# Performance work log

Hardware: AMD Instinct MI355X
Metric: run time of the kernel (lower is better)

The kernel has to match this reference:

```python
import jax, jax.numpy as jnp
import numpy as np
import math

B, S, D, H = 4, 1024, 1024, 16
HD = D // H  # 64
DFF = 4 * D
LN_EPS = 1e-5

def setup_inputs() -> dict:
    key = jax.random.key(0)
    ks = jax.random.split(key, 24)
    sd = lambda fi, fo: 1.0 / math.sqrt(fi)
    def lin(k, fi, fo):
        k1, k2 = jax.random.split(k)
        w = jax.random.uniform(k1, (fi, fo), jnp.float32, -sd(fi, fo), sd(fi, fo))
        b = jax.random.uniform(k2, (fo,), jnp.float32, -sd(fi, fo), sd(fi, fo))
        return w, b
    x = jax.random.normal(ks[0], (B, S, D), jnp.float32)
    Wk, bk = lin(ks[1], D, D)
    Wq, bq = lin(ks[2], D, D)
    Wv, bv = lin(ks[3], D, D)
    # per-head projections stacked over heads: [H, D, HD]
    def head_lin(k):
        kk = jax.random.split(k, H)
        ws, bs = zip(*[lin(kk[h], D, HD) for h in range(H)])
        return jnp.stack(ws), jnp.stack(bs)
    Whq, bhq = head_lin(ks[4])
    Whk, bhk = head_lin(ks[5])
    Whv, bhv = head_lin(ks[6])
    Wo, bo = lin(ks[7], D, D)
    W1, b1 = lin(ks[8], D, DFF)
    W2, b2 = lin(ks[9], DFF, D)
    gamma = jnp.ones((D,), jnp.float32)
    beta = jnp.zeros((D,), jnp.float32)
    return dict(x=x, Wk=Wk, bk=bk, Wq=Wq, bq=bq, Wv=Wv, bv=bv,
                Whq=Whq, bhq=bhq, Whk=Whk, bhk=bhk, Whv=Whv, bhv=bhv,
                Wo=Wo, bo=bo, W1=W1, b1=b1, W2=W2, b2=b2,
                gamma=gamma, beta=beta)

def _layer_norm(x, gamma, beta):
    mu = jnp.mean(x, axis=-1, keepdims=True)
    var = jnp.mean(jnp.square(x - mu), axis=-1, keepdims=True)
    return (x - mu) * jax.lax.rsqrt(var + LN_EPS) * gamma + beta

def reference(x, Wk, bk, Wq, bq, Wv, bv, Whq, bhq, Whk, bhk, Whv, bhv,
              Wo, bo, W1, b1, W2, b2, gamma, beta):
    # outer projections; NOTE: forward passes (k, q, v) into MHA, so the
    # MHA 'Q' stream is k_proj(x), 'K' stream is q_proj(x), 'V' is v_proj(x)
    ko = x @ Wk + bk
    qo = x @ Wq + bq
    vo = x @ Wv + bv
    # per-head projections (batched over heads): [B,H,S,HD]
    q = jnp.einsum('bsd,hde->bhse', ko, Whq) + bhq[None, :, None, :]
    k = jnp.einsum('bsd,hde->bhse', qo, Whk) + bhk[None, :, None, :]
    v = jnp.einsum('bsd,hde->bhse', vo, Whv) + bhv[None, :, None, :]
    # NOTE: original scales by sqrt(d_model), not sqrt(head_dim)
    scores = jnp.einsum('bhse,bhte->bhst', q, k) / math.sqrt(D)
    w = jax.nn.softmax(scores, axis=-1)
    o = jnp.einsum('bhst,bhte->bhse', w, v)         # [B,H,S,HD]
    o = o.transpose(0, 2, 1, 3).reshape(B, S, D)    # concat heads
    attn = o @ Wo + bo
    # dropout is identity in eval; shared LayerNorm after both residuals
    r1 = _layer_norm(x + attn, gamma, beta)
    ff = jax.nn.gelu(r1 @ W1 + b1, approximate=False) @ W2 + b2
    out = _layer_norm(r1 + ff, gamma, beta)
    return out
```

## Files before the change

kernel.cpp:

```cpp
#include <hip/hip_runtime.h>
#include <cstdint>
#include <cstddef>

#define D_MODEL 1024
#define SEQ 1024
#define BATCH 4
#define NHEAD 16
#define HDIM 64
#define ROWS (BATCH*SEQ)

typedef unsigned short u16;
typedef __attribute__((ext_vector_type(4))) unsigned short u16x4;
typedef __attribute__((ext_vector_type(8))) unsigned short u16x8;
typedef __attribute__((ext_vector_type(8))) __bf16 bf16x8v;
typedef __attribute__((ext_vector_type(4))) float f32x4;

__device__ inline u16 f2bf(float f){
  union{float f; unsigned u;} c; c.f = f;
  unsigned r = c.u + 0x7FFFu + ((c.u>>16)&1u);
  return (u16)(r>>16);
}
__device__ inline float bf2f(u16 s){
  union{unsigned u; float f;} c; c.u = ((unsigned)s)<<16; return c.f;
}
__device__ inline float gelu_f(float x){ return 0.5f*x*(1.f+erff(x*0.7071067811865475f)); }

__device__ __forceinline__ void gload_lds16(const void* g, void* l){
  __builtin_amdgcn_global_load_lds(
    (const __attribute__((address_space(1))) unsigned int*)g,
    (__attribute__((address_space(3))) unsigned int*)l, 16, 0, 0);
}

__global__ __launch_bounds__(256) void convert_bf(const float* __restrict__ in, u16* __restrict__ out){
  size_t idx = (size_t)blockIdx.x*256 + threadIdx.x;
  f32x4 v = *(const f32x4*)(in + idx*4);
  u16x4 o = { f2bf(v.x), f2bf(v.y), f2bf(v.z), f2bf(v.w) };
  *(u16x4*)(out + idx*4) = o;
}

__global__ __launch_bounds__(256) void transpose_conv(const float* __restrict__ W, u16* __restrict__ WT, int K, int N){
  __shared__ float tile[32][33];
  int n0 = blockIdx.x*32, k0 = blockIdx.y*32;
  int tx = threadIdx.x & 31, ty = threadIdx.x >> 5;
  #pragma unroll
  for (int i=0;i<4;i++){
    int r = ty + i*8;
    tile[r][tx] = W[(size_t)(k0+r)*N + n0 + tx];
  }
  __syncthreads();
  #pragma unroll
  for (int i=0;i<4;i++){
    int r = ty + i*8;
    WT[(size_t)(n0+r)*K + k0 + tx] = f2bf(tile[tx][r]);
  }
}

__global__ __launch_bounds__(256) void head_transpose(const float* __restrict__ Wh, u16* __restrict__ WT){
  __shared__ float tile[32][33];
  int d0 = blockIdx.x*32, e0 = blockIdx.y*32, h = blockIdx.z;
  int tx = threadIdx.x & 31, ty = threadIdx.x >> 5;
  #pragma unroll
  for (int i=0;i<4;i++){
    int r = ty + i*8;
    tile[r][tx] = Wh[(size_t)h*D_MODEL*HDIM + (size_t)(d0+r)*HDIM + e0 + tx];
  }
  __syncthreads();
  #pragma unroll
  for (int i=0;i<4;i++){
    int r = ty + i*8;
    WT[(size_t)(h*HDIM + e0 + r)*D_MODEL + d0 + tx] = f2bf(tile[tx][r]);
  }
}

__global__ __launch_bounds__(256) void bias_cat(const float* a, const float* b, const float* c, float* o){
  int i = blockIdx.x*256 + threadIdx.x;
  float v = (i < 1024) ? a[i] : (i < 2048) ? b[i-1024] : c[i-2048];
  o[i] = v;
}

__global__ __launch_bounds__(512,2) void gemm256_8p(
  const u16* __restrict__ A, const u16* __restrict__ BT, const float* __restrict__ bias,
  u16* __restrict__ outB, int N, int K, int mode, int act)
{
  __shared__ __align__(16) u16 As[2][2][128*64];
  __shared__ __align__(16) u16 Bs[2][2][128*64];
  int t = threadIdx.x, lane = t&63, wid = t>>6;
  int wr = wid>>2, wc = wid&3;
  int fr = lane&15, kg = lane>>4;
  int gx = gridDim.x;
  int bid = blockIdx.y*gx + blockIdx.x;
  int nwg = gx*gridDim.y;
  int cpx = nwg>>3;
  int sw = (bid&7)*cpx + (bid>>3);
  int tc = sw % gx, tr = sw / gx;

  const u16* Abase = A  + (size_t)tr*256*K;
  const u16* Bbase = BT + (size_t)tc*256*K;
  int srow = lane>>3, sch8 = lane&7;

  f32x4 acc[8][4];
  #pragma unroll
  for (int m=0;m<8;m++)
    #pragma unroll
    for (int n=0;n<4;n++) acc[m][n] = (f32x4)0.f;

  bf16x8v af[2][4], bfv[2][2];

  #define STAGE_A8(buf,h,kt) { _Pragma("unroll") for (int li=0;li<2;li++){ \
    int sr = (wid*2+li)*8 + srow; \
    int gr = ((sr>>6)<<7) + (h)*64 + (sr&63); \
    int sc = sch8 ^ (sr&7); \
    gload_lds16(Abase + (size_t)gr*K + (size_t)(kt)*64 + sc*8, &As[buf][h][(wid*2+li)*512]); } }
  #define STAGE_B8(buf,h,kt) { _Pragma("unroll") for (int li=0;li<2;li++){ \
    int sr = (wid*2+li)*8 + srow; \
    int gc = ((sr>>5)<<6) + (h)*32 + (sr&31); \
    int sc = sch8 ^ (sr&7); \
    gload_lds16(Bbase + (size_t)gc*K + (size_t)(kt)*64 + sc*8, &Bs[buf][h][(wid*2+li)*512]); } }
  #define LDA8(buf,h) { _Pragma("unroll") for (int ks=0;ks<2;ks++) _Pragma("unroll") for (int mf=0;mf<4;mf++){ \
    int r = wr*64 + mf*16 + fr; \
    af[ks][mf] = *(const bf16x8v*)&As[buf][h][r*64 + (((kg+4*ks)^(r&7)))*8]; } }
  #define LDB8(buf,h) { _Pragma("unroll") for (int ks=0;ks<2;ks++) _Pragma("unroll") for (int nf=0;nf<2;nf++){ \
    int r = wc*32 + nf*16 + fr; \
    bfv[ks][nf] = *(const bf16x8v*)&Bs[buf][h][r*64 + (((kg+4*ks)^(r&7)))*8]; } }
  #define MM8(mq,nq) { asm volatile("s_waitcnt lgkmcnt(0)" ::: "memory"); \
    __builtin_amdgcn_s_setprio(1); \
    _Pragma("unroll") for (int ks=0;ks<2;ks++) _Pragma("unroll") for (int mf=0;mf<4;mf++) _Pragma("unroll") for (int nf=0;nf<2;nf++) \
      acc[(mq)*4+mf][(nq)*2+nf] = __builtin_amdgcn_mfma_f32_16x16x32_bf16(af[ks][mf], bfv[ks][nf], acc[(mq)*4+mf][(nq)*2+nf], 0,0,0); \
    __builtin_amdgcn_s_setprio(0); }
  #define BAR asm volatile("s_barrier" ::: "memory")

  int NT = K >> 6;
  STAGE_A8(0,0,0); STAGE_B8(0,0,0); STAGE_B8(0,1,0); STAGE_A8(0,1,0);
  asm volatile("s_waitcnt vmcnt(4)" ::: "memory");
  BAR;

  for (int kt=0; kt<NT; ++kt){
    int buf = kt&1, nb = buf^1;
    int pre = (kt+1 < NT);
    LDA8(buf,0); LDB8(buf,0);
    if (pre){ STAGE_A8(nb,0,kt+1); asm volatile("s_waitcnt vmcnt(4)" ::: "memory"); }
    else    {                      asm volatile("s_waitcnt vmcnt(2)" ::: "memory"); }
    BAR; MM8(0,0); BAR;
    LDB8(buf,1);
    if (pre){ STAGE_B8(nb,0,kt+1); asm volatile("s_waitcnt vmcnt(4)" ::: "memory"); }
    else    {                      asm volatile("s_waitcnt vmcnt(0)" ::: "memory"); }
    BAR; MM8(0,1); BAR;
    LDA8(buf,1);
    if (pre){ STAGE_B8(nb,1,kt+1); asm volatile("s_waitcnt vmcnt(6)" ::: "memory"); }
    BAR; MM8(1,1); BAR;
    LDB8(buf,0);
    if (pre){ STAGE_A8(nb,1,kt+1); asm volatile("s_waitcnt vmcnt(4)" ::: "memory"); }
    BAR; MM8(1,0); BAR;
  }

  int crow0 = tr*256 + wr*128;
  int ccol0 = tc*256 + wc*64;
  #pragma unroll
  for (int n=0;n<4;n++){
    int col = ccol0 + n*16 + fr;
    float bv = bias[mode==0 ? col : (col & (N-1))];
    #pragma unroll
    for (int m=0;m<8;m++){
      int rbase = crow0 + m*16 + kg*4;
      #pragma unroll
      for (int i=0;i<4;i++){
        float v = acc[m][n][i] + bv;
        if (act) v = gelu_f(v);
        int row = rbase + i;
        if (mode == 0)
          outB[(size_t)(col>>10)*((size_t)ROWS*1024) + (size_t)row*1024 + (col&1023)] = f2bf(v);
        else
          outB[(size_t)row*N + col] = f2bf(v);
      }
    }
  }
}

__device__ __forceinline__ void stage128(u16 (*As)[4096], u16 (*Bs)[4096], int b,
  const u16* Ab, const u16* Bb, int Kstride, int kt, int wid, int rr, int sch)
{
  #pragma unroll
  for (int c=0;c<2;c++){
    int reg = c*4 + wid;
    int row = reg*16 + rr;
    gload_lds16(Ab + (size_t)row*Kstride + kt*32 + sch*8, &As[b][reg*512]);
  }
  #pragma unroll
  for (int c=0;c<2;c++){
    int reg = c*4 + wid;
    int row = reg*16 + rr;
    gload_lds16(Bb + (size_t)row*Kstride + kt*32 + sch*8, &Bs[b][reg*512]);
  }
}

__device__ __forceinline__ void gemm128_core(u16 (*As)[4096], u16 (*Bs)[4096],
  const u16* __restrict__ A, const u16* __restrict__ BT, const float* __restrict__ bias,
  float* __restrict__ outF, u16* __restrict__ outB,
  int N, int Kstride, int kofs, int Ksub, int mode, int act, int addbias)
{
  int t = threadIdx.x, lane = t&63, wid = t>>6;
  int wr = wid>>1, wc = wid&1;
  int fr = lane&15, kg = lane>>4;
  int gx = gridDim.x;
  int bid = blockIdx.y*gx + blockIdx.x;
  int nwg = gx*gridDim.y;
// ... 33 lines not shown
    for (int m=0;m<4;m++){
      int r = wr*64 + m*16 + fr;
      af[m] = *(const bf16x8v*)&As[buf][r*32 + (kg ^ ((r>>1)&3))*8];
    }
    #pragma unroll
    for (int n=0;n<4;n++){
      int r = wc*64 + n*16 + fr;
      bfv[n] = *(const bf16x8v*)&Bs[buf][r*32 + (kg ^ ((r>>1)&3))*8];
    }
    #pragma unroll
    for (int m=0;m<4;m++)
      #pragma unroll
      for (int n=0;n<4;n++)
        acc[m][n] = __builtin_amdgcn_mfma_f32_16x16x32_bf16(af[m], bfv[n], acc[m][n], 0,0,0);
    if (kt+1 < NT)
      asm volatile("s_barrier" ::: "memory");
    buf += 1; if (buf >= 3) buf = 0;
  }

  int crow0 = tr*128 + wr*64;
  int ccol0 = tc*128 + wc*64;
  #pragma unroll
  for (int n=0;n<4;n++){
    int col = ccol0 + n*16 + fr;
    float bv = addbias ? bias[col] : 0.f;
    #pragma unroll
    for (int m=0;m<4;m++){
      int rbase = crow0 + m*16 + kg*4;
      #pragma unroll
      for (int i=0;i<4;i++){
        float v = acc[m][n][i] + bv;
        if (act) v = gelu_f(v);
        int row = rbase + i;
        if (mode == 0){
          outB[(size_t)(col>>10)*((size_t)ROWS*1024) + (size_t)row*1024 + (col&1023)] = f2bf(v);
        } else if (mode == 1){
          outB[(size_t)row*N + col] = f2bf(v);
        } else if (mode == 2){
          int b = row >> 10, s = row & 1023;
          int h = col >> 6, e = col & 63;
          outB[(((size_t)((b*NHEAD + h)*HDIM + e))<<10) + s] = f2bf(v);
        } else {
          outF[(size_t)row*1024 + col] = v;
        }
      }
    }
  }
}

__global__ __launch_bounds__(256) void g_gemm_sk(
  const u16* A, const u16* BT, const float* bias, float* outBase, int K)
{
  __shared__ __align__(16) u16 As[3][4096];
  __shared__ __align__(16) u16 Bs[3][4096];
  int z = blockIdx.z;
  int Ksub = K >> 1;
  gemm128_core(As, Bs, A, BT, bias, outBase + (size_t)z*ROWS*1024, nullptr,
               1024, K, z*Ksub, Ksub, 3, 0, z==0);
}

struct B3 { const u16* A[3]; const u16* BT[3]; const float* bias[3]; u16* Cb[3]; int mode[3]; };
__global__ __launch_bounds__(256) void g_gemm_b3(B3 p){
  __shared__ __align__(16) u16 As[3][4096];
  __shared__ __align__(16) u16 Bs[3][4096];
  int z = blockIdx.z;
  gemm128_core(As, Bs, p.A[z], p.BT[z], p.bias[z], nullptr, p.Cb[z],
               1024, 1024, 0, 1024, p.mode[z], 0, 1);
}

__global__ __launch_bounds__(256) void attn_mfma(const u16* __restrict__ Q, const u16* __restrict__ Km,
                                                 const u16* __restrict__ Vt, u16* __restrict__ O)
{
  __shared__ __align__(16) u16 Ks[64*64];
  __shared__ __align__(16) u16 Vs[64*64];
  __shared__ __align__(16) u16 Ps[4][16*64];
  int t = threadIdx.x, lane = t & 63, wid = t >> 6;
  int fr = lane & 15, kg = lane >> 4;
  int qt = blockIdx.x, h = blockIdx.y, b = blockIdx.z;
  const size_t qkbase = ((size_t)b*SEQ)*D_MODEL + (size_t)h*HDIM;
  const size_t vtb = ((size_t)(b*NHEAD + h))*HDIM*SEQ;

  int qrow = qt*64 + wid*16 + fr;
  bf16x8v aq[2];
  aq[0] = *(const bf16x8v*)(Q + qkbase + (size_t)qrow*D_MODEL + kg*8);
  aq[1] = *(const bf16x8v*)(Q + qkbase + (size_t)qrow*D_MODEL + 32 + kg*8);

  f32x4 Oacc[4];
  #pragma unroll
  for (int n=0;n<4;n++) Oacc[n] = (f32x4)0.f;
  float m_run[4], l_run[4];
  #pragma unroll
  for (int i=0;i<4;i++){ m_run[i] = -3e38f; l_run[i] = 0.f; }

  int srow = lane >> 3;
  int sch  = (lane & 7) ^ srow;
  int x7 = fr & 7;

  for (int kt = 0; kt < SEQ/64; ++kt){
    #pragma unroll
    for (int c=0;c<2;c++){
      int r0 = (wid*2 + c)*8;
      int rowk = r0 + srow;
      gload_lds16(Km + qkbase + (size_t)(kt*64 + rowk)*D_MODEL + sch*8, &Ks[r0*64]);
      gload_lds16(Vt + vtb + (size_t)rowk*SEQ + kt*64 + sch*8, &Vs[r0*64]);
    }
    __syncthreads();

    f32x4 z4 = (f32x4)0.f;
    f32x4 s4[4];
    #pragma unroll
    for (int n=0;n<4;n++){
      int r = n*16 + fr;
      bf16x8v k0v = *(const bf16x8v*)&Ks[r*64 + ((kg  ) ^ x7)*8];
      bf16x8v k1v = *(const bf16x8v*)&Ks[r*64 + ((4+kg) ^ x7)*8];
      s4[n] = __builtin_amdgcn_mfma_f32_16x16x32_bf16(aq[0], k0v, z4, 0,0,0);
      s4[n] = __builtin_amdgcn_mfma_f32_16x16x32_bf16(aq[1], k1v, s4[n], 0,0,0);
      s4[n] *= 0.03125f;
    }

    float mI[4], sc[4], ls[4], p[4][4];
    #pragma unroll
    for (int i=0;i<4;i++)
      mI[i] = fmaxf(fmaxf(s4[0][i], s4[1][i]), fmaxf(s4[2][i], s4[3][i]));
    #pragma unroll
    for (int off=1; off<16; off<<=1){
      #pragma unroll
      for (int i=0;i<4;i++) mI[i] = fmaxf(mI[i], __shfl_xor(mI[i], off));
    }
    #pragma unroll
    for (int i=0;i<4;i++){
      float m_new = fmaxf(m_run[i], mI[i]);
      sc[i] = __expf(m_run[i] - m_new);
      m_run[i] = m_new;
      ls[i] = 0.f;
    }
    #pragma unroll
    for (int n=0;n<4;n++)
      #pragma unroll
      for (int i=0;i<4;i++){
        float pv = __expf(s4[n][i] - m_run[i]);
        p[n][i] = pv;
        ls[i] += pv;
      }
    #pragma unroll
    for (int off=1; off<16; off<<=1){
      #pragma unroll
      for (int i=0;i<4;i++) ls[i] += __shfl_xor(ls[i], off);
    }
    #pragma unroll
    for (int i=0;i<4;i++) l_run[i] = l_run[i]*sc[i] + ls[i];
    #pragma unroll
    for (int n=0;n<4;n++)
      #pragma unroll
      for (int i=0;i<4;i++) Oacc[n][i] *= sc[i];

    u16* Pw = &Ps[wid][0];
    #pragma unroll
    for (int n=0;n<4;n++){
      int chunk = n*2 + (fr>>3);
      #pragma unroll
      for (int i=0;i<4;i++){
        int row = kg*4 + i;
        Pw[row*64 + (chunk ^ (row&7))*8 + (fr&7)] = f2bf(p[n][i]);
      }
    }
    asm volatile("s_waitcnt lgkmcnt(0)" ::: "memory");

    bf16x8v ap0 = *(const bf16x8v*)&Pw[fr*64 + ((kg  ) ^ x7)*8];
    bf16x8v ap1 = *(const bf16x8v*)&Pw[fr*64 + ((4+kg) ^ x7)*8];
    #pragma unroll
    for (int n2=0;n2<4;n2++){
      int r = n2*16 + fr;
      bf16x8v v0 = *(const bf16x8v*)&Vs[r*64 + ((kg  ) ^ x7)*8];
      bf16x8v v1 = *(const bf16x8v*)&Vs[r*64 + ((4+kg) ^ x7)*8];
      Oacc[n2] = __builtin_amdgcn_mfma_f32_16x16x32_bf16(ap0, v0, Oacc[n2], 0,0,0);
      Oacc[n2] = __builtin_amdgcn_mfma_f32_16x16x32_bf16(ap1, v1, Oacc[n2], 0,0,0);
    }
    __syncthreads();
  }

  float inv[4];
  #pragma unroll
  for (int i=0;i<4;i++) inv[i] = 1.f / l_run[i];
  #pragma unroll
  for (int n2=0;n2<4;n2++){
    #pragma unroll
    for (int i=0;i<4;i++){
      int row = qt*64 + wid*16 + kg*4 + i;
      O[qkbase + (size_t)row*D_MODEL + n2*16 + fr] = f2bf(Oacc[n2][i]*inv[i]);
    }
  }
}

__global__ __launch_bounds__(256) void ln_sum3(const float* __restrict__ A, const float* __restrict__ B,
   const float* __restrict__ C, const float* __restrict__ gamma, const float* __restrict__ beta,
   float* __restrict__ Of, u16* __restrict__ Ob)
{
  int row = blockIdx.x, t = threadIdx.x;
  size_t base = (size_t)row*D_MODEL + t*4;
  f32x4 v = *(const f32x4*)(A + base);
  v += *(const f32x4*)(B + base);
  v += *(const f32x4*)(C + base);
  float s = v.x+v.y+v.z+v.w;
  float q = v.x*v.x+v.y*v.y+v.z*v.z+v.w*v.w;
  #pragma unroll
  for (int off=1; off<64; off<<=1){ s += __shfl_xor(s,off); q += __shfl_xor(q,off); }
  __shared__ float red[8];
  int wid = t>>6;
  if ((t&63)==0){ red[wid] = s; red[wid+4] = q; }
  __syncthreads();
  s = red[0]+red[1]+red[2]+red[3];
  q = red[4]+red[5]+red[6]+red[7];
  float mu = s*(1.f/1024.f);
  float var = q*(1.f/1024.f) - mu*mu;
  float rs = rsqrtf(var + 1e-5f);
  f32x4 g4 = *(const f32x4*)(gamma + t*4);
  f32x4 b4 = *(const f32x4*)(beta + t*4);
  f32x4 o;
  o.x = (v.x-mu)*rs*g4.x + b4.x;
  o.y = (v.y-mu)*rs*g4.y + b4.y;
  o.z = (v.z-mu)*rs*g4.z + b4.z;
  o.w = (v.w-mu)*rs*g4.w + b4.w;
// ... 2 lines not shown
    u16x4 ob = { f2bf(o.x), f2bf(o.y), f2bf(o.z), f2bf(o.w) };
    *(u16x4*)(Ob + base) = ob;
  }
}

extern "C" void kernel_launch(void* const* d_in, const int* in_sizes, int n_in,
                              void* d_out, int out_size, void* d_ws, size_t ws_size,
                              hipStream_t stream)
{
  const float* x    = (const float*)d_in[0];
  const float* Wk   = (const float*)d_in[1];
  const float* bk   = (const float*)d_in[2];
  const float* Wq   = (const float*)d_in[3];
  const float* bq   = (const float*)d_in[4];
  const float* Wv   = (const float*)d_in[5];
  const float* bv   = (const float*)d_in[6];
  const float* Whq  = (const float*)d_in[7];
  const float* bhq  = (const float*)d_in[8];
  const float* Whk  = (const float*)d_in[9];
  const float* bhk  = (const float*)d_in[10];
  const float* Whv  = (const float*)d_in[11];
  const float* bhv  = (const float*)d_in[12];
  const float* Wo   = (const float*)d_in[13];
  const float* bo   = (const float*)d_in[14];
  const float* W1   = (const float*)d_in[15];
  const float* b1   = (const float*)d_in[16];
  const float* W2   = (const float*)d_in[17];
  const float* b2   = (const float*)d_in[18];
  const float* gamma= (const float*)d_in[19];
  const float* beta = (const float*)d_in[20];

  char* ws = (char*)d_ws;
  const size_t MB_ = 1024*1024;
  u16* WkT  = (u16*)(ws + 0*MB_);
  u16* WqT  = (u16*)(ws + 2*MB_);
  u16* WvT  = (u16*)(ws + 4*MB_);
  u16* WhqT = (u16*)(ws + 6*MB_);
  u16* WhkT = (u16*)(ws + 8*MB_);
  u16* WhvT = (u16*)(ws + 10*MB_);
  u16* WoT  = (u16*)(ws + 12*MB_);
  u16* W1T  = (u16*)(ws + 14*MB_);
  u16* W2T  = (u16*)(ws + 22*MB_);
  u16* xb   = (u16*)(ws + 30*MB_);
  u16* kob  = (u16*)(ws + 38*MB_);
  u16* qob  = (u16*)(ws + 46*MB_);
  u16* vob  = (u16*)(ws + 54*MB_);
  u16* qb   = (u16*)(ws + 62*MB_);
  u16* kb   = (u16*)(ws + 70*MB_);
  u16* vt   = (u16*)(ws + 78*MB_);
  u16* Ob   = (u16*)(ws + 86*MB_);
  u16* ff1b = (u16*)(ws + 38*MB_);
  float* r1f = (float*)(ws + 70*MB_);
  u16*  r1b  = (u16*)(ws + 86*MB_);
  float* P0  = (float*)(ws + 94*MB_);
  float* P1  = (float*)(ws + 110*MB_);
  float* bcat = (float*)(ws + 126*MB_);

  dim3 tb(256);

  convert_bf<<<dim3(ROWS*D_MODEL/4/256), tb, 0, stream>>>(x, xb);
  transpose_conv<<<dim3(32,32),  tb, 0, stream>>>(Wk, WkT, 1024, 1024);
  transpose_conv<<<dim3(32,32),  tb, 0, stream>>>(Wq, WqT, 1024, 1024);
  transpose_conv<<<dim3(32,32),  tb, 0, stream>>>(Wv, WvT, 1024, 1024);
  transpose_conv<<<dim3(32,32),  tb, 0, stream>>>(Wo, WoT, 1024, 1024);
  transpose_conv<<<dim3(128,32), tb, 0, stream>>>(W1, W1T, 1024, 4096);
  transpose_conv<<<dim3(32,128), tb, 0, stream>>>(W2, W2T, 4096, 1024);
  head_transpose<<<dim3(32,2,16), tb, 0, stream>>>(Whq, WhqT);
  head_transpose<<<dim3(32,2,16), tb, 0, stream>>>(Whk, WhkT);
  head_transpose<<<dim3(32,2,16), tb, 0, stream>>>(Whv, WhvT);
  bias_cat<<<dim3(12), tb, 0, stream>>>(bk, bq, bv, bcat);

  gemm256_8p<<<dim3(12,16), dim3(512), 0, stream>>>(xb, WkT, bcat, kob, 3072, 1024, 0, 0);

  B3 p2;
  p2.A[0]=kob; p2.A[1]=qob; p2.A[2]=vob;
  p2.BT[0]=WhqT; p2.BT[1]=WhkT; p2.BT[2]=WhvT;
  p2.bias[0]=bhq; p2.bias[1]=bhk; p2.bias[2]=bhv;
  p2.Cb[0]=qb; p2.Cb[1]=kb; p2.Cb[2]=vt;
  p2.mode[0]=1; p2.mode[1]=1; p2.mode[2]=2;
  g_gemm_b3<<<dim3(8,32,3), tb, 0, stream>>>(p2);

  attn_mfma<<<dim3(16,16,4), tb, 0, stream>>>(qb, kb, vt, Ob);

  g_gemm_sk<<<dim3(8,32,2), tb, 0, stream>>>(Ob, WoT, bo, P0, 1024);
  ln_sum3<<<dim3(4096), tb, 0, stream>>>(x, P0, P1, gamma, beta, r1f, r1b);
  gemm256_8p<<<dim3(16,16), dim3(512), 0, stream>>>(r1b, W1T, b1, ff1b, 4096, 1024, 1, 1);
  g_gemm_sk<<<dim3(8,32,2), tb, 0, stream>>>(ff1b, W2T, b2, P0, 4096);
  ln_sum3<<<dim3(4096), tb, 0, stream>>>(r1f, P0, P1, gamma, beta, (float*)d_out, nullptr);

  (void)in_sizes; (void)n_in; (void)out_size; (void)ws_size;
}
```

Baseline: 333.6 us.

## Rework attention kernel with 32-row waves, direct K/V loads, lazy rescale

The attention kernel now gives each wave 32 query rows (two 16-row fragments) and 128 rows per block, halving the grid. K and V fragments are read straight from global memory into registers instead of being staged through LDS, which removes the block-wide barriers. Softmax uses exp2 with a prefolded scale and rescales the running max only when it grows by more than 8, which skips most rescale multiplies at the cost of slightly looser numerical headroom. Separately, the 256-tile GEMM core keeps two B-fragment register sets so the fourth B LDS reload per k-step is dropped, adding register pressure.

```diff
diff --git a/kernel.cpp b/kernel.cpp
--- a/kernel.cpp
+++ b/kernel.cpp
@@ -104,7 +104,7 @@
     #pragma unroll
     for (int n=0;n<4;n++) acc[m][n] = (f32x4)0.f;
 
-  bf16x8v af[2][4], bfv[2][2];
+  bf16x8v af[2][4], bv0[2][2], bv1[2][2];
 
   #define STAGE_A8(buf,h,kt) { _Pragma("unroll") for (int li=0;li<2;li++){ \
     int sr = (wid*2+li)*8 + srow; \
@@ -119,13 +119,13 @@
   #define LDA8(buf,h) { _Pragma("unroll") for (int ks=0;ks<2;ks++) _Pragma("unroll") for (int mf=0;mf<4;mf++){ \
     int r = wr*64 + mf*16 + fr; \
     af[ks][mf] = *(const bf16x8v*)&As[buf][h][r*64 + (((kg+4*ks)^(r&7)))*8]; } }
-  #define LDB8(buf,h) { _Pragma("unroll") for (int ks=0;ks<2;ks++) _Pragma("unroll") for (int nf=0;nf<2;nf++){ \
+  #define LDB8(buf,h,dst) { _Pragma("unroll") for (int ks=0;ks<2;ks++) _Pragma("unroll") for (int nf=0;nf<2;nf++){ \
     int r = wc*32 + nf*16 + fr; \
-    bfv[ks][nf] = *(const bf16x8v*)&Bs[buf][h][r*64 + (((kg+4*ks)^(r&7)))*8]; } }
-  #define MM8(mq,nq) { asm volatile("s_waitcnt lgkmcnt(0)" ::: "memory"); \
+    dst[ks][nf] = *(const bf16x8v*)&Bs[buf][h][r*64 + (((kg+4*ks)^(r&7)))*8]; } }
+  #define MM8(mq,nq,bv) { asm volatile("s_waitcnt lgkmcnt(0)" ::: "memory"); \
     __builtin_amdgcn_s_setprio(1); \
     _Pragma("unroll") for (int ks=0;ks<2;ks++) _Pragma("unroll") for (int mf=0;mf<4;mf++) _Pragma("unroll") for (int nf=0;nf<2;nf++) \
-      acc[(mq)*4+mf][(nq)*2+nf] = __builtin_amdgcn_mfma_f32_16x16x32_bf16(af[ks][mf], bfv[ks][nf], acc[(mq)*4+mf][(nq)*2+nf], 0,0,0); \
+      acc[(mq)*4+mf][(nq)*2+nf] = __builtin_amdgcn_mfma_f32_16x16x32_bf16(af[ks][mf], bv[ks][nf], acc[(mq)*4+mf][(nq)*2+nf], 0,0,0); \
     __builtin_amdgcn_s_setprio(0); }
   #define BAR asm volatile("s_barrier" ::: "memory")
 
@@ -137,20 +137,19 @@
   for (int kt=0; kt<NT; ++kt){
     int buf = kt&1, nb = buf^1;
     int pre = (kt+1 < NT);
-    LDA8(buf,0); LDB8(buf,0);
+    LDA8(buf,0); LDB8(buf,0,bv0);
     if (pre){ STAGE_A8(nb,0,kt+1); asm volatile("s_waitcnt vmcnt(4)" ::: "memory"); }
     else    {                      asm volatile("s_waitcnt vmcnt(2)" ::: "memory"); }
-    BAR; MM8(0,0); BAR;
-    LDB8(buf,1);
+    BAR; MM8(0,0,bv0); BAR;
+    LDB8(buf,1,bv1);
     if (pre){ STAGE_B8(nb,0,kt+1); asm volatile("s_waitcnt vmcnt(4)" ::: "memory"); }
     else    {                      asm volatile("s_waitcnt vmcnt(0)" ::: "memory"); }
-    BAR; MM8(0,1); BAR;
+    BAR; MM8(0,1,bv1); BAR;
     LDA8(buf,1);
     if (pre){ STAGE_B8(nb,1,kt+1); asm volatile("s_waitcnt vmcnt(6)" ::: "memory"); }
-    BAR; MM8(1,1); BAR;
-    LDB8(buf,0);
+    BAR; MM8(1,1,bv1); BAR;
     if (pre){ STAGE_A8(nb,1,kt+1); asm volatile("s_waitcnt vmcnt(4)" ::: "memory"); }
-    BAR; MM8(1,0); BAR;
+    BAR; MM8(1,0,bv0); BAR;
   }
 
   int crow0 = tr*256 + wr*128;
@@ -309,123 +308,131 @@
 __global__ __launch_bounds__(256) void attn_mfma(const u16* __restrict__ Q, const u16* __restrict__ Km,
                                                  const u16* __restrict__ Vt, u16* __restrict__ O)
 {
-  __shared__ __align__(16) u16 Ks[64*64];
-  __shared__ __align__(16) u16 Vs[64*64];
-  __shared__ __align__(16) u16 Ps[4][16*64];
+  __shared__ __align__(16) u16 Ps[4][32*64];
   int t = threadIdx.x, lane = t & 63, wid = t >> 6;
   int fr = lane & 15, kg = lane >> 4;
   int qt = blockIdx.x, h = blockIdx.y, b = blockIdx.z;
   const size_t qkbase = ((size_t)b*SEQ)*D_MODEL + (size_t)h*HDIM;
   const size_t vtb = ((size_t)(b*NHEAD + h))*HDIM*SEQ;
-
-  int qrow = qt*64 + wid*16 + fr;
-  bf16x8v aq[2];
-  aq[0] = *(const bf16x8v*)(Q + qkbase + (size_t)qrow*D_MODEL + kg*8);
-  aq[1] = *(const bf16x8v*)(Q + qkbase + (size_t)qrow*D_MODEL + 32 + kg*8);
-
-  f32x4 Oacc[4];
-  #pragma unroll
-  for (int n=0;n<4;n++) Oacc[n] = (f32x4)0.f;
-  float m_run[4], l_run[4];
-  #pragma unroll
-  for (int i=0;i<4;i++){ m_run[i] = -3e38f; l_run[i] = 0.f; }
-
-  int srow = lane >> 3;
-  int sch  = (lane & 7) ^ srow;
+  int qbase = qt*128 + wid*32;
   int x7 = fr & 7;
 
+  bf16x8v aq[2][2];
+  #pragma unroll
+  for (int mq=0;mq<2;mq++){
+    const u16* qp = Q + qkbase + (size_t)(qbase + mq*16 + fr)*D_MODEL;
+    aq[mq][0] = *(const bf16x8v*)(qp + kg*8);
+    aq[mq][1] = *(const bf16x8v*)(qp + 32 + kg*8);
+  }
+
+  f32x4 Oacc[2][4];
+  float m2[2][4], lr[2][4];
+  #pragma unroll
+  for (int mq=0;mq<2;mq++){
+    #pragma unroll
+    for (int n=0;n<4;n++) Oacc[mq][n] = (f32x4)0.f;
+    #pragma unroll
+    for (int i=0;i<4;i++){ m2[mq][i] = -3e38f; lr[mq][i] = 0.f; }
+  }
+
+  const float CS = 0.03125f * 1.4426950408889634f;
+  u16* Pw = &Ps[wid][0];
+
   for (int kt = 0; kt < SEQ/64; ++kt){
-    #pragma unroll
-    for (int c=0;c<2;c++){
-      int r0 = (wid*2 + c)*8;
-      int rowk = r0 + srow;
-      gload_lds16(Km + qkbase + (size_t)(kt*64 + rowk)*D_MODEL + sch*8, &Ks[r0*64]);
-      gload_lds16(Vt + vtb + (size_t)rowk*SEQ + kt*64 + sch*8, &Vs[r0*64]);
-    }
-    __syncthreads();
-
-    f32x4 z4 = (f32x4)0.f;
-    f32x4 s4[4];
+    f32x4 s4[2][4];
     #pragma unroll
     for (int n=0;n<4;n++){
-      int r = n*16 + fr;
-      bf16x8v k0v = *(const bf16x8v*)&Ks[r*64 + ((kg  ) ^ x7)*8];
-      bf16x8v k1v = *(const bf16x8v*)&Ks[r*64 + ((4+kg) ^ x7)*8];
-      s4[n] = __builtin_amdgcn_mfma_f32_16x16x32_bf16(aq[0], k0v, z4, 0,0,0);
-      s4[n] = __builtin_amdgcn_mfma_f32_16x16x32_bf16(aq[1], k1v, s4[n], 0,0,0);
-      s4[n] *= 0.03125f;
-    }
-
-    float mI[4], sc[4], ls[4], p[4][4];
-    #pragma unroll
-    for (int i=0;i<4;i++)
-      mI[i] = fmaxf(fmaxf(s4[0][i], s4[1][i]), fmaxf(s4[2][i], s4[3][i]));
-    #pragma unroll
-    for (int off=1; off<16; off<<=1){
-      #pragma unroll
-      for (int i=0;i<4;i++) mI[i] = fmaxf(mI[i], __shfl_xor(mI[i], off));
-    }
+      const u16* kp = Km + qkbase + (size_t)(kt*64 + n*16 + fr)*D_MODEL;
+      bf16x8v k0 = *(const bf16x8v*)(kp + kg*8);
+      bf16x8v k1 = *(const bf16x8v*)(kp + 32 + kg*8);
+      #pragma unroll
+      for (int mq=0;mq<2;mq++){
+        f32x4 z = (f32x4)0.f;
+        z = __builtin_amdgcn_mfma_f32_16x16x32_bf16(aq[mq][0], k0, z, 0,0,0);
+        s4[mq][n] = __builtin_amdgcn_mfma_f32_16x16x32_bf16(aq[mq][1], k1, z, 0,0,0);
+      }
+    }
+    #pragma unroll
+    for (int mq=0;mq<2;mq++)
+      #pragma unroll
+      for (int n=0;n<4;n++) s4[mq][n] *= CS;
+
+    #pragma unroll
+    for (int mq=0;mq<2;mq++){
+      float mI[4];
+      #pragma unroll
+      for (int i=0;i<4;i++)
+        mI[i] = fmaxf(fmaxf(s4[mq][0][i], s4[mq][1][i]), fmaxf(s4[mq][2][i], s4[mq][3][i]));
+      #pragma unroll
+      for (int off=1; off<16; off<<=1){
+        #pragma unroll
+        for (int i=0;i<4;i++) mI[i] = fmaxf(mI[i], __shfl_xor(mI[i], off));
+      }
+      float g = -3e38f;
+      #pragma unroll
+      for (int i=0;i<4;i++) g = fmaxf(g, mI[i] - m2[mq][i]);
+      if (__any(g > 8.f)){
+        #pragma unroll
+        for (int i=0;i<4;i++){
+          float mn = fmaxf(m2[mq][i], mI[i]);
+          float sc = exp2f(m2[mq][i] - mn);
+          m2[mq][i] = mn;
+          lr[mq][i] *= sc;
+          #pragma unroll
+          for (int n=0;n<4;n++) Oacc[mq][n][i] *= sc;
+        }
+      }
+      float ls[4] = {0.f,0.f,0.f,0.f};
+      #pragma unroll
+      for (int n=0;n<4;n++){
+        int chunk = n*2 + (fr>>3);
+        #pragma unroll
+        for (int i=0;i<4;i++){
+          float pv = exp2f(s4[mq][n][i] - m2[mq][i]);
+          ls[i] += pv;
+          int row = mq*16 + kg*4 + i;
+          Pw[row*64 + (chunk ^ (row&7))*8 + (fr&7)] = f2bf(pv);
+        }
+      }
+      #pragma unroll
+      for (int off=1; off<16; off<<=1){
+        #pragma unroll
+        for (int i=0;i<4;i++) ls[i] += __shfl_xor(ls[i], off);
+      }
+      #pragma unroll
+      for (int i=0;i<4;i++) lr[mq][i] += ls[i];
+    }
+    asm volatile("s_waitcnt lgkmcnt(0)" ::: "memory");
+
+    bf16x8v ap[2][2];
+    #pragma unroll
+    for (int mq=0;mq<2;mq++){
+      int rr = mq*16 + fr;
+      ap[mq][0] = *(const bf16x8v*)&Pw[rr*64 + ((kg  ) ^ x7)*8];
+      ap[mq][1] = *(const bf16x8v*)&Pw[rr*64 + ((4+kg) ^ x7)*8];
+    }
+    #pragma unroll
+    for (int n2=0;n2<4;n2++){
+      const u16* vp = Vt + vtb + (size_t)(n2*16+fr)*SEQ + (size_t)kt*64;
+      bf16x8v v0 = *(const bf16x8v*)(vp + kg*8);
+      bf16x8v v1 = *(const bf16x8v*)(vp + 32 + kg*8);
+      #pragma unroll
+      for (int mq=0;mq<2;mq++){
+        Oacc[mq][n2] = __builtin_amdgcn_mfma_f32_16x16x32_bf16(ap[mq][0], v0, Oacc[mq][n2], 0,0,0);
+        Oacc[mq][n2] = __builtin_amdgcn_mfma_f32_16x16x32_bf16(ap[mq][1], v1, Oacc[mq][n2], 0,0,0);
+      }
+    }
+  }
+
+  #pragma unroll
+  for (int mq=0;mq<2;mq++){
     #pragma unroll
     for (int i=0;i<4;i++){
-      float m_new = fmaxf(m_run[i], mI[i]);
-      sc[i] = __expf(m_run[i] - m_new);
-      m_run[i] = m_new;
-      ls[i] = 0.f;
-    }
-    #pragma unroll
-    for (int n=0;n<4;n++)
-      #pragma unroll
-      for (int i=0;i<4;i++){
-        float pv = __expf(s4[n][i] - m_run[i]);
-        p[n][i] = pv;
-        ls[i] += pv;
-      }
-    #pragma unroll
-    for (int off=1; off<16; off<<=1){
-      #pragma unroll
-      for (int i=0;i<4;i++) ls[i] += __shfl_xor(ls[i], off);
-    }
-    #pragma unroll
-    for (int i=0;i<4;i++) l_run[i] = l_run[i]*sc[i] + ls[i];
-    #pragma unroll
-    for (int n=0;n<4;n++)
-      #pragma unroll
-      for (int i=0;i<4;i++) Oacc[n][i] *= sc[i];
-
-    u16* Pw = &Ps[wid][0];
-    #pragma unroll
-    for (int n=0;n<4;n++){
-      int chunk = n*2 + (fr>>3);
-      #pragma unroll
-      for (int i=0;i<4;i++){
-        int row = kg*4 + i;
-        Pw[row*64 + (chunk ^ (row&7))*8 + (fr&7)] = f2bf(p[n][i]);
-      }
-    }
-    asm volatile("s_waitcnt lgkmcnt(0)" ::: "memory");
-
-    bf16x8v ap0 = *(const bf16x8v*)&Pw[fr*64 + ((kg  ) ^ x7)*8];
-    bf16x8v ap1 = *(const bf16x8v*)&Pw[fr*64 + ((4+kg) ^ x7)*8];
-    #pragma unroll
-    for (int n2=0;n2<4;n2++){
-      int r = n2*16 + fr;
-      bf16x8v v0 = *(const bf16x8v*)&Vs[r*64 + ((kg  ) ^ x7)*8];
-      bf16x8v v1 = *(const bf16x8v*)&Vs[r*64 + ((4+kg) ^ x7)*8];
-      Oacc[n2] = __builtin_amdgcn_mfma_f32_16x16x32_bf16(ap0, v0, Oacc[n2], 0,0,0);
-      Oacc[n2] = __builtin_amdgcn_mfma_f32_16x16x32_bf16(ap1, v1, Oacc[n2], 0,0,0);
-    }
-    __syncthreads();
-  }
-
-  float inv[4];
-  #pragma unroll
-  for (int i=0;i<4;i++) inv[i] = 1.f / l_run[i];
-  #pragma unroll
-  for (int n2=0;n2<4;n2++){
-    #pragma unroll
-    for (int i=0;i<4;i++){
-      int row = qt*64 + wid*16 + kg*4 + i;
-      O[qkbase + (size_t)row*D_MODEL + n2*16 + fr] = f2bf(Oacc[n2][i]*inv[i]);
+      float inv = 1.f / lr[mq][i];
+      int row = qbase + mq*16 + kg*4 + i;
+      #pragma unroll
+      for (int n2=0;n2<4;n2++)
+        O[qkbase + (size_t)row*D_MODEL + n2*16 + fr] = f2bf(Oacc[mq][n2][i]*inv);
     }
   }
 }
@@ -542,7 +549,7 @@
   p2.mode[0]=1; p2.mode[1]=1; p2.mode[2]=2;
   g_gemm_b3<<<dim3(8,32,3), tb, 0, stream>>>(p2);
 
-  attn_mfma<<<dim3(16,16,4), tb, 0, stream>>>(qb, kb, vt, Ob);
+  attn_mfma<<<dim3(8,16,4), tb, 0, stream>>>(qb, kb, vt, Ob);
 
   g_gemm_sk<<<dim3(8,32,2), tb, 0, stream>>>(Ob, WoT, bo, P0, 1024);
   ln_sum3<<<dim3(4096), tb, 0, stream>>>(x, P0, P1, gamma, beta, r1f, r1b);
```

Result: slower. 341.6 us (+2.4%).

## Fold outer and per-head projections into one combined weight GEMM, pipeline attention

Applied to the files above, without the earlier changes.

Precomposes each outer projection weight with its per-head weights (W·Wh) and folds the biases (b·Wh + bh), so the two chained projection GEMMs over activations become one 4096x3072x1024 GEMM whose epilogue writes Q, K and the transposed V directly. The weight-combining GEMM is small and runs on weights only. The attention kernel also gains double-buffered K/V staging, exp2-based softmax with lazy rescaling (only when the max grows by more than a threshold), and the scale folded into one constant. The big GEMM keeps two B register sets to avoid a reload. Together these remove a full activation GEMM pass and its intermediates, at the cost of more bf16 rounding in the composed weights.

```diff
diff --git a/kernel.cpp b/kernel.cpp
--- a/kernel.cpp
+++ b/kernel.cpp
@@ -38,6 +38,15 @@
   *(u16x4*)(out + idx*4) = o;
 }
 
+struct C3 { const float* src[3]; u16* dst[3]; };
+__global__ __launch_bounds__(256) void convert_w3(C3 p){
+  int z = blockIdx.z;
+  size_t idx = (size_t)blockIdx.x*256 + threadIdx.x;
+  f32x4 v = *(const f32x4*)(p.src[z] + idx*4);
+  u16x4 o = { f2bf(v.x), f2bf(v.y), f2bf(v.z), f2bf(v.w) };
+  *(u16x4*)(p.dst[z] + idx*4) = o;
+}
+
 __global__ __launch_bounds__(256) void transpose_conv(const float* __restrict__ W, u16* __restrict__ WT, int K, int N){
   __shared__ float tile[32][33];
   int n0 = blockIdx.x*32, k0 = blockIdx.y*32;
@@ -55,9 +64,13 @@
   }
 }
 
-__global__ __launch_bounds__(256) void head_transpose(const float* __restrict__ Wh, u16* __restrict__ WT){
+struct H3 { const float* src[3]; u16* dst[3]; };
+__global__ __launch_bounds__(256) void head_transpose3(H3 p){
   __shared__ float tile[32][33];
-  int d0 = blockIdx.x*32, e0 = blockIdx.y*32, h = blockIdx.z;
+  int z = blockIdx.z; int which = z >> 4; int h = z & 15;
+  const float* Wh = p.src[which];
+  u16* WT = p.dst[which];
+  int d0 = blockIdx.x*32, e0 = blockIdx.y*32;
   int tx = threadIdx.x & 31, ty = threadIdx.x >> 5;
   #pragma unroll
   for (int i=0;i<4;i++){
@@ -72,10 +85,19 @@
   }
 }
 
-__global__ __launch_bounds__(256) void bias_cat(const float* a, const float* b, const float* c, float* o){
-  int i = blockIdx.x*256 + threadIdx.x;
-  float v = (i < 1024) ? a[i] : (i < 2048) ? b[i-1024] : c[i-2048];
-  o[i] = v;
+__global__ __launch_bounds__(64) void bias_comb(
+  const float* bk, const float* bq, const float* bv,
+  const float* Whq, const float* Whk, const float* Whv,
+  const float* bhq, const float* bhk, const float* bhv, float* bc)
+{
+  int blk = blockIdx.x; int which = blk >> 4; int h = blk & 15; int e = threadIdx.x;
+  const float* bvec = (which==0) ? bk : (which==1) ? bq : bv;
+  const float* Wh   = (which==0) ? Whq : (which==1) ? Whk : Whv;
+  const float* bh   = (which==0) ? bhq : (which==1) ? bhk : bhv;
+  float s = bh[h*HDIM + e];
+  const float* w = Wh + (size_t)h*D_MODEL*HDIM + e;
+  for (int d=0; d<D_MODEL; ++d) s += bvec[d] * w[(size_t)d*HDIM];
+  bc[which*1024 + h*HDIM + e] = s;
 }
 
 __global__ __launch_bounds__(512,2) void gemm256_8p(
@@ -104,7 +126,7 @@
     #pragma unroll
     for (int n=0;n<4;n++) acc[m][n] = (f32x4)0.f;
 
-  bf16x8v af[2][4], bfv[2][2];
+  bf16x8v af[2][4], bv0[2][2], bv1[2][2];
 
   #define STAGE_A8(buf,h,kt) { _Pragma("unroll") for (int li=0;li<2;li++){ \
     int sr = (wid*2+li)*8 + srow; \
@@ -119,13 +141,13 @@
   #define LDA8(buf,h) { _Pragma("unroll") for (int ks=0;ks<2;ks++) _Pragma("unroll") for (int mf=0;mf<4;mf++){ \
     int r = wr*64 + mf*16 + fr; \
     af[ks][mf] = *(const bf16x8v*)&As[buf][h][r*64 + (((kg+4*ks)^(r&7)))*8]; } }
-  #define LDB8(buf,h) { _Pragma("unroll") for (int ks=0;ks<2;ks++) _Pragma("unroll") for (int nf=0;nf<2;nf++){ \
+  #define LDB8(buf,h,dst) { _Pragma("unroll") for (int ks=0;ks<2;ks++) _Pragma("unroll") for (int nf=0;nf<2;nf++){ \
     int r = wc*32 + nf*16 + fr; \
-    bfv[ks][nf] = *(const bf16x8v*)&Bs[buf][h][r*64 + (((kg+4*ks)^(r&7)))*8]; } }
-  #define MM8(mq,nq) { asm volatile("s_waitcnt lgkmcnt(0)" ::: "memory"); \
+    dst[ks][nf] = *(const bf16x8v*)&Bs[buf][h][r*64 + (((kg+4*ks)^(r&7)))*8]; } }
+  #define MM8(mq,nq,bv) { asm volatile("s_waitcnt lgkmcnt(0)" ::: "memory"); \
     __builtin_amdgcn_s_setprio(1); \
     _Pragma("unroll") for (int ks=0;ks<2;ks++) _Pragma("unroll") for (int mf=0;mf<4;mf++) _Pragma("unroll") for (int nf=0;nf<2;nf++) \
-      acc[(mq)*4+mf][(nq)*2+nf] = __builtin_amdgcn_mfma_f32_16x16x32_bf16(af[ks][mf], bfv[ks][nf], acc[(mq)*4+mf][(nq)*2+nf], 0,0,0); \
+      acc[(mq)*4+mf][(nq)*2+nf] = __builtin_amdgcn_mfma_f32_16x16x32_bf16(af[ks][mf], bv[ks][nf], acc[(mq)*4+mf][(nq)*2+nf], 0,0,0); \
     __builtin_amdgcn_s_setprio(0); }
   #define BAR asm volatile("s_barrier" ::: "memory")
 
@@ -137,20 +159,19 @@
   for (int kt=0; kt<NT; ++kt){
     int buf = kt&1, nb = buf^1;
     int pre = (kt+1 < NT);
-    LDA8(buf,0); LDB8(buf,0);
+    LDA8(buf,0); LDB8(buf,0,bv0);
     if (pre){ STAGE_A8(nb,0,kt+1); asm volatile("s_waitcnt vmcnt(4)" ::: "memory"); }
     else    {                      asm volatile("s_waitcnt vmcnt(2)" ::: "memory"); }
-    BAR; MM8(0,0); BAR;
-    LDB8(buf,1);
+    BAR; MM8(0,0,bv0); BAR;
+    LDB8(buf,1,bv1);
     if (pre){ STAGE_B8(nb,0,kt+1); asm volatile("s_waitcnt vmcnt(4)" ::: "memory"); }
     else    {                      asm volatile("s_waitcnt vmcnt(0)" ::: "memory"); }
-    BAR; MM8(0,1); BAR;
+    BAR; MM8(0,1,bv1); BAR;
     LDA8(buf,1);
     if (pre){ STAGE_B8(nb,1,kt+1); asm volatile("s_waitcnt vmcnt(6)" ::: "memory"); }
-    BAR; MM8(1,1); BAR;
-    LDB8(buf,0);
+    BAR; MM8(1,1,bv1); BAR;
     if (pre){ STAGE_A8(nb,1,kt+1); asm volatile("s_waitcnt vmcnt(4)" ::: "memory"); }
-    BAR; MM8(1,0); BAR;
+    BAR; MM8(1,0,bv0); BAR;
   }
 
   int crow0 = tr*256 + wr*128;
@@ -158,7 +179,7 @@
   #pragma unroll
   for (int n=0;n<4;n++){
     int col = ccol0 + n*16 + fr;
-    float bv = bias[mode==0 ? col : (col & (N-1))];
+    float bv = bias[col];
     #pragma unroll
     for (int m=0;m<8;m++){
       int rbase = crow0 + m*16 + kg*4;
@@ -167,10 +188,18 @@
         float v = acc[m][n][i] + bv;
         if (act) v = gelu_f(v);
         int row = rbase + i;
-        if (mode == 0)
-          outB[(size_t)(col>>10)*((size_t)ROWS*1024) + (size_t)row*1024 + (col&1023)] = f2bf(v);
-        else
+        if (mode == 1){
           outB[(size_t)row*N + col] = f2bf(v);
+        } else {
+          int panel = col >> 10, c1 = col & 1023;
+          if (panel < 2)
+            outB[(size_t)panel*((size_t)ROWS*1024) + (size_t)row*1024 + c1] = f2bf(v);
+          else {
+            int b = row >> 10, s = row & 1023;
+            int hh = c1 >> 6, e = c1 & 63;
+            outB[(size_t)2*((size_t)ROWS*1024) + (((size_t)((b*NHEAD+hh)*HDIM+e))<<10) + s] = f2bf(v);
+          }
+        }
       }
     }
   }
@@ -270,14 +299,8 @@
         float v = acc[m][n][i] + bv;
         if (act) v = gelu_f(v);
         int row = rbase + i;
-        if (mode == 0){
-          outB[(size_t)(col>>10)*((size_t)ROWS*1024) + (size_t)row*1024 + (col&1023)] = f2bf(v);
-        } else if (mode == 1){
+        if (mode == 1){
           outB[(size_t)row*N + col] = f2bf(v);
-        } else if (mode == 2){
-          int b = row >> 10, s = row & 1023;
-          int h = col >> 6, e = col & 63;
-          outB[(((size_t)((b*NHEAD + h)*HDIM + e))<<10) + s] = f2bf(v);
         } else {
           outF[(size_t)row*1024 + col] = v;
         }
@@ -297,20 +320,20 @@
                1024, K, z*Ksub, Ksub, 3, 0, z==0);
 }
 
-struct B3 { const u16* A[3]; const u16* BT[3]; const float* bias[3]; u16* Cb[3]; int mode[3]; };
-__global__ __launch_bounds__(256) void g_gemm_b3(B3 p){
+struct B3 { const u16* A[3]; const u16* BT[3]; u16* Cb[3]; };
+__global__ __launch_bounds__(256) void g_gemm_b3(B3 p, const float* bias){
   __shared__ __align__(16) u16 As[3][4096];
   __shared__ __align__(16) u16 Bs[3][4096];
   int z = blockIdx.z;
-  gemm128_core(As, Bs, p.A[z], p.BT[z], p.bias[z], nullptr, p.Cb[z],
-               1024, 1024, 0, 1024, p.mode[z], 0, 1);
+  gemm128_core(As, Bs, p.A[z], p.BT[z], bias, nullptr, p.Cb[z],
+               1024, 1024, 0, 1024, 1, 0, 0);
 }
 
 __global__ __launch_bounds__(256) void attn_mfma(const u16* __restrict__ Q, const u16* __restrict__ Km,
                                                  const u16* __restrict__ Vt, u16* __restrict__ O)
 {
-  __shared__ __align__(16) u16 Ks[64*64];
-  __shared__ __align__(16) u16 Vs[64*64];
+  __shared__ __align__(16) u16 Ks[2][64*64];
+  __shared__ __align__(16) u16 Vs[2][64*64];
   __shared__ __align__(16) u16 Ps[4][16*64];
   int t = threadIdx.x, lane = t & 63, wid = t >> 6;
   int fr = lane & 15, kg = lane >> 4;
@@ -319,9 +342,8 @@
   const size_t vtb = ((size_t)(b*NHEAD + h))*HDIM*SEQ;
 
   int qrow = qt*64 + wid*16 + fr;
-  bf16x8v aq[2];
-  aq[0] = *(const bf16x8v*)(Q + qkbase + (size_t)qrow*D_MODEL + kg*8);
-  aq[1] = *(const bf16x8v*)(Q + qkbase + (size_t)qrow*D_MODEL + 32 + kg*8);
+  bf16x8v aq0 = *(const bf16x8v*)(Q + qkbase + (size_t)qrow*D_MODEL + kg*8);
+  bf16x8v aq1 = *(const bf16x8v*)(Q + qkbase + (size_t)qrow*D_MODEL + 32 + kg*8);
 
   f32x4 Oacc[4];
   #pragma unroll
@@ -333,30 +355,36 @@
   int srow = lane >> 3;
   int sch  = (lane & 7) ^ srow;
   int x7 = fr & 7;
+  const float CS = 0.03125f * 1.4426950408889634f;
+  u16* Pw = &Ps[wid][0];
+
+  #define ASTG(bf,kt) { _Pragma("unroll") for (int c=0;c<2;c++){ \
+    int r0 = (wid*2 + c)*8; int rowk = r0 + srow; \
+    gload_lds16(Km + qkbase + (size_t)((kt)*64 + rowk)*D_MODEL + sch*8, &Ks[bf][r0*64]); \
+    gload_lds16(Vt + vtb + (size_t)rowk*SEQ + (kt)*64 + sch*8, &Vs[bf][r0*64]); } }
+
+  ASTG(0,0);
+  asm volatile("s_waitcnt vmcnt(0)" ::: "memory");
+  __syncthreads();
 
   for (int kt = 0; kt < SEQ/64; ++kt){
-    #pragma unroll
-    for (int c=0;c<2;c++){
-      int r0 = (wid*2 + c)*8;
-      int rowk = r0 + srow;
-      gload_lds16(Km + qkbase + (size_t)(kt*64 + rowk)*D_MODEL + sch*8, &Ks[r0*64]);
-      gload_lds16(Vt + vtb + (size_t)rowk*SEQ + kt*64 + sch*8, &Vs[r0*64]);
-    }
-    __syncthreads();
-
-    f32x4 z4 = (f32x4)0.f;
+    int bf = kt & 1;
+    if (kt+1 < SEQ/64) ASTG(bf^1, kt+1);
+
     f32x4 s4[4];
     #pragma unroll
     for (int n=0;n<4;n++){
       int r = n*16 + fr;
-      bf16x8v k0v = *(const bf16x8v*)&Ks[r*64 + ((kg  ) ^ x7)*8];
-      bf16x8v k1v = *(const bf16x8v*)&Ks[r*64 + ((4+kg) ^ x7)*8];
-      s4[n] = __builtin_amdgcn_mfma_f32_16x16x32_bf16(aq[0], k0v, z4, 0,0,0);
-      s4[n] = __builtin_amdgcn_mfma_f32_16x16x32_bf16(aq[1], k1v, s4[n], 0,0,0);
-      s4[n] *= 0.03125f;
-    }
-
-    float mI[4], sc[4], ls[4], p[4][4];
+      bf16x8v k0 = *(const bf16x8v*)&Ks[bf][r*64 + ((kg  ) ^ x7)*8];
+      bf16x8v k1 = *(const bf16x8v*)&Ks[bf][r*64 + ((4+kg) ^ x7)*8];
+      f32x4 z = (f32x4)0.f;
+      z = __builtin_amdgcn_mfma_f32_16x16x32_bf16(aq0, k0, z, 0,0,0);
+      s4[n] = __builtin_amdgcn_mfma_f32_16x16x32_bf16(aq1, k1, z, 0,0,0);
+    }
+    #pragma unroll
+    for (int n=0;n<4;n++) s4[n] *= CS;
+
+    float mI[4];
     #pragma unroll
     for (int i=0;i<4;i++)
       mI[i] = fmaxf(fmaxf(s4[0][i], s4[1][i]), fmaxf(s4[2][i], s4[3][i]));
@@ -365,43 +393,39 @@
       #pragma unroll
       for (int i=0;i<4;i++) mI[i] = fmaxf(mI[i], __shfl_xor(mI[i], off));
     }
-    #pragma unroll
-    for (int i=0;i<4;i++){
-      float m_new = fmaxf(m_run[i], mI[i]);
-      sc[i] = __expf(m_run[i] - m_new);
-      m_run[i] = m_new;
-      ls[i] = 0.f;
-    }
-    #pragma unroll
-    for (int n=0;n<4;n++)
+    float g = -3e38f;
+    #pragma unroll
+    for (int i=0;i<4;i++) g = fmaxf(g, mI[i] - m_run[i]);
+    if (__any(g > 8.f)){
       #pragma unroll
       for (int i=0;i<4;i++){
-        float pv = __expf(s4[n][i] - m_run[i]);
-        p[n][i] = pv;
-        ls[i] += pv;
+        float mn = fmaxf(m_run[i], mI[i]);
+        float sc = exp2f(m_run[i] - mn);
+        m_run[i] = mn;
+        l_run[i] *= sc;
+        #pragma unroll
+        for (int n=0;n<4;n++) Oacc[n][i] *= sc;
       }
-    #pragma unroll
-    for (int off=1; off<16; off<<=1){
-      #pragma unroll
-      for (int i=0;i<4;i++) ls[i] += __shfl_xor(ls[i], off);
-    }
-    #pragma unroll
-    for (int i=0;i<4;i++) l_run[i] = l_run[i]*sc[i] + ls[i];
-    #pragma unroll
-    for (int n=0;n<4;n++)
-      #pragma unroll
-      for (int i=0;i<4;i++) Oacc[n][i] *= sc[i];
-
-    u16* Pw = &Ps[wid][0];
+    }
+    float ls[4] = {0.f,0.f,0.f,0.f};
     #pragma unroll
     for (int n=0;n<4;n++){
       int chunk = n*2 + (fr>>3);
       #pragma unroll
       for (int i=0;i<4;i++){
+        float pv = exp2f(s4[n][i] - m_run[i]);
+        ls[i] += pv;
         int row = kg*4 + i;
-        Pw[row*64 + (chunk ^ (row&7))*8 + (fr&7)] = f2bf(p[n][i]);
+        Pw[row*64 + (chunk ^ (row&7))*8 + (fr&7)] = f2bf(pv);
       }
     }
+    #pragma unroll
+    for (int off=1; off<16; off<<=1){
+      #pragma unroll
+      for (int i=0;i<4;i++) ls[i] += __shfl_xor(ls[i], off);
+    }
+    #pragma unroll
+    for (int i=0;i<4;i++) l_run[i] += ls[i];
     asm volatile("s_waitcnt lgkmcnt(0)" ::: "memory");
 
     bf16x8v ap0 = *(const bf16x8v*)&Pw[fr*64 + ((kg  ) ^ x7)*8];
@@ -409,11 +433,12 @@
     #pragma unroll
     for (int n2=0;n2<4;n2++){
       int r = n2*16 + fr;
-      bf16x8v v0 = *(const bf16x8v*)&Vs[r*64 + ((kg  ) ^ x7)*8];
-      bf16x8v v1 = *(const bf16x8v*)&Vs[r*64 + ((4+kg) ^ x7)*8];
+      bf16x8v v0 = *(const bf16x8v*)&Vs[bf][r*64 + ((kg  ) ^ x7)*8];
+      bf16x8v v1 = *(const bf16x8v*)&Vs[bf][r*64 + ((4+kg) ^ x7)*8];
       Oacc[n2] = __builtin_amdgcn_mfma_f32_16x16x32_bf16(ap0, v0, Oacc[n2], 0,0,0);
       Oacc[n2] = __builtin_amdgcn_mfma_f32_16x16x32_bf16(ap1, v1, Oacc[n2], 0,0,0);
     }
+    asm volatile("s_waitcnt vmcnt(0)" ::: "memory");
     __syncthreads();
   }
 
@@ -494,9 +519,9 @@
 
   char* ws = (char*)d_ws;
   const size_t MB_ = 1024*1024;
-  u16* WkT  = (u16*)(ws + 0*MB_);
-  u16* WqT  = (u16*)(ws + 2*MB_);
-  u16* WvT  = (u16*)(ws + 4*MB_);
+  u16* Wkb  = (u16*)(ws + 0*MB_);
+  u16* Wqb  = (u16*)(ws + 2*MB_);
+  u16* Wvb  = (u16*)(ws + 4*MB_);
   u16* WhqT = (u16*)(ws + 6*MB_);
   u16* WhkT = (u16*)(ws + 8*MB_);
   u16* WhvT = (u16*)(ws + 10*MB_);
@@ -504,51 +529,47 @@
   u16* W1T  = (u16*)(ws + 14*MB_);
   u16* W2T  = (u16*)(ws + 22*MB_);
   u16* xb   = (u16*)(ws + 30*MB_);
-  u16* kob  = (u16*)(ws + 38*MB_);
-  u16* qob  = (u16*)(ws + 46*MB_);
-  u16* vob  = (u16*)(ws + 54*MB_);
-  u16* qb   = (u16*)(ws + 62*MB_);
-  u16* kb   = (u16*)(ws + 70*MB_);
-  u16* vt   = (u16*)(ws + 78*MB_);
-  u16* Ob   = (u16*)(ws + 86*MB_);
-  u16* ff1b = (u16*)(ws + 38*MB_);
-  float* r1f = (float*)(ws + 70*MB_);
-  u16*  r1b  = (u16*)(ws + 86*MB_);
-  float* P0  = (float*)(ws + 94*MB_);
-  float* P1  = (float*)(ws + 110*MB_);
-  float* bcat = (float*)(ws + 126*MB_);
+  u16* WcT  = (u16*)(ws + 38*MB_);
+  float* bc = (float*)(ws + 44*MB_);
+  u16* qb   = (u16*)(ws + 46*MB_);
+  u16* kb   = (u16*)(ws + 54*MB_);
+  u16* vt   = (u16*)(ws + 62*MB_);
+  u16* Ob   = (u16*)(ws + 70*MB_);
+  float* Pa = (float*)(ws + 78*MB_);
+  float* Pb = (float*)(ws + 94*MB_);
+  float* r1f = (float*)(ws + 110*MB_);
+  u16*  r1b  = (u16*)(ws + 38*MB_);
+  u16*  ff1b = (u16*)(ws + 46*MB_);
 
   dim3 tb(256);
 
   convert_bf<<<dim3(ROWS*D_MODEL/4/256), tb, 0, stream>>>(x, xb);
-  transpose_conv<<<dim3(32,32),  tb, 0, stream>>>(Wk, WkT, 1024, 1024);
-  transpose_conv<<<dim3(32,32),  tb, 0, stream>>>(Wq, WqT, 1024, 1024);
-  transpose_conv<<<dim3(32,32),  tb, 0, stream>>>(Wv, WvT, 1024, 1024);
+  C3 cw; cw.src[0]=Wk; cw.src[1]=Wq; cw.src[2]=Wv;
+  cw.dst[0]=Wkb; cw.dst[1]=Wqb; cw.dst[2]=Wvb;
+  convert_w3<<<dim3(1024,1,3), tb, 0, stream>>>(cw);
+  H3 hh; hh.src[0]=Whq; hh.src[1]=Whk; hh.src[2]=Whv;
+  hh.dst[0]=WhqT; hh.dst[1]=WhkT; hh.dst[2]=WhvT;
+  head_transpose3<<<dim3(32,2,48), tb, 0, stream>>>(hh);
   transpose_conv<<<dim3(32,32),  tb, 0, stream>>>(Wo, WoT, 1024, 1024);
   transpose_conv<<<dim3(128,32), tb, 0, stream>>>(W1, W1T, 1024, 4096);
   transpose_conv<<<dim3(32,128), tb, 0, stream>>>(W2, W2T, 4096, 1024);
-  head_transpose<<<dim3(32,2,16), tb, 0, stream>>>(Whq, WhqT);
-  head_transpose<<<dim3(32,2,16), tb, 0, stream>>>(Whk, WhkT);
-  head_transpose<<<dim3(32,2,16), tb, 0, stream>>>(Whv, WhvT);
-  bias_cat<<<dim3(12), tb, 0, stream>>>(bk, bq, bv, bcat);
-
-  gemm256_8p<<<dim3(12,16), dim3(512), 0, stream>>>(xb, WkT, bcat, kob, 3072, 1024, 0, 0);
-
-  B3 p2;
-  p2.A[0]=kob; p2.A[1]=qob; p2.A[2]=vob;
-  p2.BT[0]=WhqT; p2.BT[1]=WhkT; p2.BT[2]=WhvT;
-  p2.bias[0]=bhq; p2.bias[1]=bhk; p2.bias[2]=bhv;
-  p2.Cb[0]=qb; p2.Cb[1]=kb; p2.Cb[2]=vt;
-  p2.mode[0]=1; p2.mode[1]=1; p2.mode[2]=2;
-  g_gemm_b3<<<dim3(8,32,3), tb, 0, stream>>>(p2);
+  bias_comb<<<dim3(48), dim3(64), 0, stream>>>(bk,bq,bv, Whq,Whk,Whv, bhq,bhk,bhv, bc);
+
+  B3 cmb;
+  cmb.A[0]=WhqT; cmb.A[1]=WhkT; cmb.A[2]=WhvT;
+  cmb.BT[0]=Wkb; cmb.BT[1]=Wqb; cmb.BT[2]=Wvb;
+  cmb.Cb[0]=WcT; cmb.Cb[1]=WcT+1048576; cmb.Cb[2]=WcT+2097152;
+  g_gemm_b3<<<dim3(8,8,3), tb, 0, stream>>>(cmb, bk);
+
+  gemm256_8p<<<dim3(12,16), dim3(512), 0, stream>>>(xb, WcT, bc, qb, 3072, 1024, 2, 0);
 
   attn_mfma<<<dim3(16,16,4), tb, 0, stream>>>(qb, kb, vt, Ob);
 
-  g_gemm_sk<<<dim3(8,32,2), tb, 0, stream>>>(Ob, WoT, bo, P0, 1024);
-  ln_sum3<<<dim3(4096), tb, 0, stream>>>(x, P0, P1, gamma, beta, r1f, r1b);
+  g_gemm_sk<<<dim3(8,32,2), tb, 0, stream>>>(Ob, WoT, bo, Pa, 1024);
+  ln_sum3<<<dim3(4096), tb, 0, stream>>>(x, Pa, Pb, gamma, beta, r1f, r1b);
   gemm256_8p<<<dim3(16,16), dim3(512), 0, stream>>>(r1b, W1T, b1, ff1b, 4096, 1024, 1, 1);
-  g_gemm_sk<<<dim3(8,32,2), tb, 0, stream>>>(ff1b, W2T, b2, P0, 4096);
-  ln_sum3<<<dim3(4096), tb, 0, stream>>>(r1f, P0, P1, gamma, beta, (float*)d_out, nullptr);
+  g_gemm_sk<<<dim3(8,32,2), tb, 0, stream>>>(ff1b, W2T, b2, Pa, 4096);
+  ln_sum3<<<dim3(4096), tb, 0, stream>>>(r1f, Pa, Pb, gamma, beta, (float*)d_out, nullptr);
 
   (void)in_sizes; (void)n_in; (void)out_size; (void)ws_size;
 }
```

New measurement: 355.8 us. 6.7% more time.
